# Kernel optimization log

Hardware: AMD Instinct MI355X
Metric: run time of the kernel (lower is better)

## Reference

```python
import math
import jax, jax.numpy as jnp
import numpy as np

B, N, E, H = 1, 4096, 256, 8
D = E // H  # head dim = 32


def setup_inputs() -> dict:
    key = jax.random.key(0)
    ks = jax.random.split(key, 10)
    s = 1.0 / math.sqrt(E)
    return {
        "x": jax.random.normal(ks[0], (B, N, E), dtype=jnp.float32),
        "adjacency": jax.random.randint(ks[1], (B, N, N), 0, 2, dtype=jnp.int32),
        "Wq": jax.random.normal(ks[2], (E, E), dtype=jnp.float32) * s,
        "bq": jnp.zeros((E,), dtype=jnp.float32),
        "Wk": jax.random.normal(ks[3], (E, E), dtype=jnp.float32) * s,
        "bk": jnp.zeros((E,), dtype=jnp.float32),
        "Wv": jax.random.normal(ks[4], (E, E), dtype=jnp.float32) * s,
        "bv": jnp.zeros((E,), dtype=jnp.float32),
        "Wo": jax.random.normal(ks[5], (E, E), dtype=jnp.float32) * s,
        "bo": jnp.zeros((E,), dtype=jnp.float32),
    }


def reference(x, adjacency, Wq, bq, Wk, bk, Wv, bv, Wo, bo):
    b, n, e = x.shape
    # projections (torch Linear: x @ W.T + b), split into heads -> [B,H,N,D]
    def heads(y):
        return y.reshape(b, n, H, D).transpose(0, 2, 1, 3)
    q = heads(x @ Wq.T + bq)
    k = heads(x @ Wk.T + bk)
    v = heads(x @ Wv.T + bv)
    scores = jnp.einsum("bhnd,bhmd->bhnm", q, k) / math.sqrt(D)
    mask = (adjacency[:, None, :, :] == 0)  # [B,1,N,N]
    scores = jnp.where(mask, -jnp.inf, scores)
    w = jax.nn.softmax(scores, axis=-1)
    out = jnp.einsum("bhnm,bhmd->bhnd", w, v)
    out = out.transpose(0, 2, 1, 3).reshape(b, n, e)
    return out @ Wo.T + bo
```

## Files before the change

kernel.cpp:

```cpp
#include <hip/hip_runtime.h>
#include <math.h>


#define NTOK 4096
#define EDIM 256
#define HEADS 8
#define HD 32
#define QSCALE 0.17677669529663687f
#define LOG2E 1.4426950408889634f
#define CINIT (-11.541560327111707f)

typedef __attribute__((ext_vector_type(8))) short bf16x8;
typedef __attribute__((ext_vector_type(4))) float f32x4;
typedef __attribute__((ext_vector_type(4))) unsigned long long u64x4;

static __device__ inline short f2bf(float f) {
    unsigned u = __float_as_uint(f);
    u = (u + 0x7FFFu + ((u >> 16) & 1u)) >> 16;
    return (short)u;
}
static __device__ inline unsigned packtrunc(float a, float b) {
    return __builtin_amdgcn_perm(__float_as_uint(b), __float_as_uint(a),
                                 0x07060302u);
}
static __device__ inline float sel_mask(float v, unsigned long long m) {
    float r;
    asm("v_cndmask_b32 %0, 0, %1, %2" : "=v"(r) : "v"(v), "s"(m));
    return r;
}

__global__ __launch_bounds__(256) void prep(
    const int* __restrict__ adj, unsigned long long* __restrict__ maskT,
    const float* __restrict__ x,  const float* __restrict__ Wq,
    const float* __restrict__ Wk, const float* __restrict__ Wv,
    const float* __restrict__ Wo,
    short* __restrict__ xb,  short* __restrict__ wqb,
    short* __restrict__ wkb, short* __restrict__ wvb,
    short* __restrict__ wob)
{
    const int bid = blockIdx.x;
    if (bid < 2048) {
        const int wb = bid * 4 + (threadIdx.x >> 6);
        const int l = threadIdx.x & 63;
        const int lrow = l & 15;
        const int lc4 = ((l >> 4) & 3) * 4;
#pragma unroll
        for (int i = 0; i < 8; ++i) {
            const int w = wb + i * 8192;
            const int qb = w >> 8;
            const int kt = (w >> 2) & 63;
            const int b = w & 3;
            const int row = qb * 16 + lrow;
            const int col = kt * 64 + b * 16 + lc4;
            const int4 av = *(const int4*)&adj[row * NTOK + col];
            const unsigned long long m0 = __ballot(av.x != 0);
            const unsigned long long m1 = __ballot(av.y != 0);
            const unsigned long long m2 = __ballot(av.z != 0);
            const unsigned long long m3 = __ballot(av.w != 0);
            if (l == 0) {
                unsigned long long* dst = &maskT[(size_t)w * 4];
                dst[0] = m0; dst[1] = m1; dst[2] = m2; dst[3] = m3;
            }
        }
    } else {
        const int gid = (bid - 2048) * 256 + threadIdx.x;
        const int e = gid * 4;
        const float* src; short* dst; int off;
        if (e < NTOK * EDIM) { src = x; dst = xb; off = e; }
        else {
            const int r = e - NTOK * EDIM;
            const int wsel = r >> 16;
            off = r & 65535;
            src = (wsel == 0) ? Wq : (wsel == 1) ? Wk : (wsel == 2) ? Wv : Wo;
            dst = (wsel == 0) ? wqb : (wsel == 1) ? wkb : (wsel == 2) ? wvb : wob;
        }
        float4 v = *(const float4*)&src[off];
        uint2 t;
        t.x = (unsigned short)f2bf(v.x) | ((unsigned)(unsigned short)f2bf(v.y) << 16);
        t.y = (unsigned short)f2bf(v.z) | ((unsigned)(unsigned short)f2bf(v.w) << 16);
        *(uint2*)&dst[off] = t;
    }
}

__global__ __launch_bounds__(256) void qkv_mfma(
    const short* __restrict__ xb,
    const short* __restrict__ Wqb, const short* __restrict__ Wkb,
    const short* __restrict__ Wvb,
    const float* __restrict__ bq, const float* __restrict__ bk,
    const float* __restrict__ bv,
    short* __restrict__ qo, short* __restrict__ ko, short* __restrict__ vto)
{
    const int tid = threadIdx.x;
    const int wv = tid >> 6, lane = tid & 63;
    const int grp = lane >> 4, lcol = lane & 15;
    const int wsel = blockIdx.y >> 2;
    const int n0 = (blockIdx.y & 3) << 6;
    const int m0 = blockIdx.x * 64 + wv * 16;
    const short* __restrict__ W = (wsel == 0) ? Wqb : (wsel == 1) ? Wkb : Wvb;
    const float* __restrict__ bias = (wsel == 0) ? bq : (wsel == 1) ? bk : bv;

    bf16x8 af[8];
#pragma unroll
    for (int k = 0; k < 8; ++k)
        af[k] = *(const bf16x8*)&xb[(m0 + lcol) * 256 + k * 32 + grp * 8];

    f32x4 acc[4] = {};
#pragma unroll
    for (int k = 0; k < 8; ++k) {
#pragma unroll
        for (int t = 0; t < 4; ++t) {
            const bf16x8 bt =
                *(const bf16x8*)&W[(n0 + t * 16 + lcol) * 256 + k * 32 + grp * 8];
            acc[t] = __builtin_amdgcn_mfma_f32_16x16x32_bf16(af[k], bt, acc[t], 0, 0, 0);
        }
    }
#pragma unroll
    for (int t = 0; t < 4; ++t) {
        const int feat = n0 + t * 16 + lcol;
        const float bval = bias[feat];
        const int h = feat >> 5, d = feat & 31;
        if (wsel == 2) {
            uint2 o;
            o.x = (unsigned short)f2bf(acc[t][0] + bval) |
                  ((unsigned)(unsigned short)f2bf(acc[t][1] + bval) << 16);
            o.y = (unsigned short)f2bf(acc[t][2] + bval) |
                  ((unsigned)(unsigned short)f2bf(acc[t][3] + bval) << 16);
            *(uint2*)&vto[h * (HD * NTOK) + d * NTOK + m0 + grp * 4] = o;
        } else {
            short* __restrict__ out = (wsel == 0) ? qo : ko;
            const float sc = (wsel == 0) ? (QSCALE * LOG2E) : 1.0f;
#pragma unroll
            for (int j = 0; j < 4; ++j)
                out[h * (NTOK * HD) + (m0 + grp * 4 + j) * HD + d] =
                    f2bf((acc[t][j] + bval) * sc);
        }
    }
}

__global__ __launch_bounds__(256) void attn_mfma(
    const short* __restrict__ qg, const short* __restrict__ kg,
    const short* __restrict__ vtg, const unsigned long long* __restrict__ maskT,
    float* __restrict__ o_part, float* __restrict__ l_part)
{
    const int h = blockIdx.y;
    const int split = blockIdx.z;
    const int q0 = blockIdx.x << 6;
    const short* __restrict__ Q  = qg  + h * (NTOK * HD);
    const short* __restrict__ K  = kg  + h * (NTOK * HD);
    const short* __restrict__ Vt = vtg + h * (HD * NTOK);

    __shared__ short Ks[2][64][40];
    __shared__ short Vs[2][32][72];
    __shared__ short P_lds[4][16][76];

    const int tid = threadIdx.x;
    const int wv = tid >> 6;
    const int lane = tid & 63;
    const int grp = lane >> 4;
    const int lcol = lane & 15;
    const int q0w = q0 + wv * 16;

    const int krow = tid >> 2, kc8 = (tid & 3) << 3;
    const int vrow = tid >> 3, vc8 = (tid & 7) << 3;

    const bf16x8 qfrag = *(const bf16x8*)&Q[(q0w + lcol) * HD + grp * 8];

    const int qb = __builtin_amdgcn_readfirstlane(blockIdx.x * 4 + wv);
    const unsigned long long* __restrict__ mbase = maskT + (size_t)qb * 1024;

    f32x4 ot[2] = {};
    f32x4 lacc = {};
    const f32x4 cinit = {CINIT, CINIT, CINIT, CINIT};
    bf16x8 ones;
#pragma unroll
    for (int i = 0; i < 8; ++i) ones[i] = (short)0x3F80;

    const int tps = 64 / (int)gridDim.z;
    const int kt_begin = split * tps;
    const int kt_end = kt_begin + tps;

    {
        const int k0 = kt_begin << 6;
        const int4 kr = *(const int4*)&K[(k0 + krow) * HD + kc8];
        const int4 vr = *(const int4*)&Vt[vrow * NTOK + k0 + vc8];
        *(int4*)&Ks[0][krow][kc8] = kr;
        *(int4*)&Vs[0][vrow][vc8] = vr;
    }
    __syncthreads();

    int cur = 0;
    for (int kt = kt_begin; kt < kt_end; ++kt) {
        int4 kr, vr;
        const bool has_next = (kt + 1 < kt_end);
        if (has_next) {
            const int k0n = (kt + 1) << 6;
            kr = *(const int4*)&K[(k0n + krow) * HD + kc8];
            vr = *(const int4*)&Vt[vrow * NTOK + k0n + vc8];
        }

        const u64x4* mp = (const u64x4*)(mbase + kt * 16);
        const u64x4 wa = mp[0], wb = mp[1], wc = mp[2], wd = mp[3];

        bf16x8 kf[4], vf[4];
#pragma unroll
        for (int b = 0; b < 4; ++b)
            kf[b] = *(const bf16x8*)&Ks[cur][b * 16 + lcol][grp * 8];
#pragma unroll
        for (int c = 0; c < 2; ++c) {
            vf[c * 2 + 0] = *(const bf16x8*)&Vs[cur][c * 16 + lcol][grp * 8];
            vf[c * 2 + 1] = *(const bf16x8*)&Vs[cur][c * 16 + lcol][32 + grp * 8];
        }

        f32x4 s[4];
        __builtin_amdgcn_s_setprio(1);
#pragma unroll
        for (int b = 0; b < 4; ++b)
            s[b] = __builtin_amdgcn_mfma_f32_16x16x32_bf16(
                kf[b], qfrag, cinit, 0, 0, 0);
        __builtin_amdgcn_s_setprio(0);

#pragma unroll
        for (int b = 0; b < 4; ++b) {
            const u64x4 wj = (b == 0) ? wa : (b == 1) ? wb : (b == 2) ? wc : wd;
            const float p0 = sel_mask(__builtin_amdgcn_exp2f(s[b][0]), wj[0]);
            const float p1 = sel_mask(__builtin_amdgcn_exp2f(s[b][1]), wj[1]);
            const float p2 = sel_mask(__builtin_amdgcn_exp2f(s[b][2]), wj[2]);
            const float p3 = sel_mask(__builtin_amdgcn_exp2f(s[b][3]), wj[3]);
            uint2 t;
            t.x = packtrunc(p0, p1);
            t.y = packtrunc(p2, p3);
            *(uint2*)&P_lds[wv][lcol][b * 16 + grp * 4] = t;
        }

        const uint2 pl0 = *(const uint2*)&P_lds[wv][lcol][grp * 8];
        const uint2 pl1 = *(const uint2*)&P_lds[wv][lcol][grp * 8 + 4];
        const uint2 pl2 = *(const uint2*)&P_lds[wv][lcol][32 + grp * 8];
        const uint2 pl3 = *(const uint2*)&P_lds[wv][lcol][32 + grp * 8 + 4];
        struct { uint2 a, b; } u0 = {pl0, pl1}, u1 = {pl2, pl3};
        const bf16x8 pf0 = __builtin_bit_cast(bf16x8, u0);
        const bf16x8 pf1 = __builtin_bit_cast(bf16x8, u1);

        __builtin_amdgcn_s_setprio(1);
#pragma unroll
        for (int c = 0; c < 2; ++c) {
            ot[c] = __builtin_amdgcn_mfma_f32_16x16x32_bf16(vf[c * 2 + 0], pf0, ot[c], 0, 0, 0);
            ot[c] = __builtin_amdgcn_mfma_f32_16x16x32_bf16(vf[c * 2 + 1], pf1, ot[c], 0, 0, 0);
        }
        lacc = __builtin_amdgcn_mfma_f32_16x16x32_bf16(ones, pf0, lacc, 0, 0, 0);
        lacc = __builtin_amdgcn_mfma_f32_16x16x32_bf16(ones, pf1, lacc, 0, 0, 0);
        __builtin_amdgcn_s_setprio(0);

        if (has_next) {
            *(int4*)&Ks[cur ^ 1][krow][kc8] = kr;
            *(int4*)&Vs[cur ^ 1][vrow][vc8] = vr;
        }
        __syncthreads();
        cur ^= 1;
    }

    float* __restrict__ ob = o_part + split * (NTOK * EDIM);
#pragma unroll
    for (int c = 0; c < 2; ++c) {
        float4 st;
        st.x = ot[c][0]; st.y = ot[c][1]; st.z = ot[c][2]; st.w = ot[c][3];
        *(float4*)&ob[(q0w + lcol) * EDIM + h * HD + c * 16 + grp * 4] = st;
    }
    if (grp == 0)
        l_part[split * (NTOK * HEADS) + (q0w + lcol) * HEADS + h] = lacc[0];
}

template <int NS>
__global__ __launch_bounds__(256) void out_mfma(
    const float* __restrict__ o_part, const float* __restrict__ l_part,
    const short* __restrict__ Wob, const float* __restrict__ bo,
    float* __restrict__ Y)
{
    const int tid = threadIdx.x;
    const int wv = tid >> 6, lane = tid & 63;
    const int grp = lane >> 4, lcol = lane & 15;
    const int n0 = blockIdx.y << 6;
    const int m0 = blockIdx.x * 64 + wv * 16;
    const int r = m0 + lcol;

    bf16x8 af[8];
#pragma unroll
    for (int k = 0; k < 8; ++k) {
        float4 s0 = {0.f, 0.f, 0.f, 0.f}, s1 = {0.f, 0.f, 0.f, 0.f};
        float lv = 0.f;
#pragma unroll
        for (int s = 0; s < NS; ++s) {
            const float* op = &o_part[s * (NTOK * EDIM) + r * EDIM + k * 32 + grp * 8];
            const float4 t0 = *(const float4*)op;
            const float4 t1 = *(const float4*)(op + 4);
            s0.x += t0.x; s0.y += t0.y; s0.z += t0.z; s0.w += t0.w;
            s1.x += t1.x; s1.y += t1.y; s1.z += t1.z; s1.w += t1.w;
            lv += l_part[s * (NTOK * HEADS) + r * HEADS + k];
        }
        const float inv = 1.0f / lv;
        bf16x8 t;
        t[0] = f2bf(s0.x * inv); t[1] = f2bf(s0.y * inv);
        t[2] = f2bf(s0.z * inv); t[3] = f2bf(s0.w * inv);
        t[4] = f2bf(s1.x * inv); t[5] = f2bf(s1.y * inv);
        t[6] = f2bf(s1.z * inv); t[7] = f2bf(s1.w * inv);
        af[k] = t;
    }

    f32x4 acc[4] = {};
#pragma unroll
    for (int k = 0; k < 8; ++k) {
#pragma unroll
        for (int t = 0; t < 4; ++t) {
            const bf16x8 bt =
                *(const bf16x8*)&Wob[(n0 + t * 16 + lcol) * 256 + k * 32 + grp * 8];
            acc[t] = __builtin_amdgcn_mfma_f32_16x16x32_bf16(af[k], bt, acc[t], 0, 0, 0);
        }
    }
#pragma unroll
    for (int t = 0; t < 4; ++t) {
        const float bval = bo[n0 + t * 16 + lcol];
#pragma unroll
        for (int j = 0; j < 4; ++j)
            Y[(m0 + grp * 4 + j) * EDIM + n0 + t * 16 + lcol] = acc[t][j] + bval;
    }
}

extern "C" void kernel_launch(void* const* d_in, const int* in_sizes, int n_in,
                              void* d_out, int out_size, void* d_ws, size_t ws_size,
                              hipStream_t stream) {
    (void)in_sizes; (void)n_in; (void)out_size;
    const float* x  = (const float*)d_in[0];
    const int*  adj = (const int*)d_in[1];
    const float* Wq = (const float*)d_in[2];
    const float* bq = (const float*)d_in[3];
    const float* Wk = (const float*)d_in[4];
    const float* bk = (const float*)d_in[5];
    const float* Wv = (const float*)d_in[6];
    const float* bv = (const float*)d_in[7];
    const float* Wo = (const float*)d_in[8];
    const float* bo = (const float*)d_in[9];

    char* ws = (char*)d_ws;
    short* x_bf  = (short*)(ws);
    short* q_ws  = (short*)(ws + (2u << 20));
    short* k_ws  = (short*)(ws + (4u << 20));
    short* vt_ws = (short*)(ws + (6u << 20));
    unsigned long long* maskT =
        (unsigned long long*)(ws + (8u << 20));
    short* Wq_bf = (short*)(ws + (10u << 20));
    short* Wk_bf = Wq_bf + (EDIM * EDIM);
    short* Wv_bf = Wk_bf + (EDIM * EDIM);
    short* Wo_bf = Wv_bf + (EDIM * EDIM);
    float* l_part = (float*)(ws + (11u << 20));
    float* o_part = (float*)(ws + (12u << 20));

    const int ns = (ws_size >= (28u << 20)) ? 4 : 2;

    prep<<<dim3(2048 + 1280), 256, 0, stream>>>(
        adj, maskT, x, Wq, Wk, Wv, Wo, x_bf, Wq_bf, Wk_bf, Wv_bf, Wo_bf);
    qkv_mfma<<<dim3(64, 12), 256, 0, stream>>>(x_bf, Wq_bf, Wk_bf, Wv_bf,
                                               bq, bk, bv, q_ws, k_ws, vt_ws);
    attn_mfma<<<dim3(64, HEADS, ns), 256, 0, stream>>>(
        q_ws, k_ws, vt_ws, maskT, o_part, l_part);
    if (ns == 4)
        out_mfma<4><<<dim3(64, 4), 256, 0, stream>>>(o_part, l_part, Wo_bf, bo,
                                                     (float*)d_out);
    else
        out_mfma<2><<<dim3(64, 4), 256, 0, stream>>>(o_part, l_part, Wo_bf, bo,
                                                     (float*)d_out);
}
```

Measured before the change: 183.6 us.

## Stage K/V tiles via direct global-to-LDS loads with XOR swizzle; fix split at 2

```diff
diff --git a/kernel.cpp b/kernel.cpp
--- a/kernel.cpp
+++ b/kernel.cpp
@@ -6,6 +6,7 @@
 #define EDIM 256
 #define HEADS 8
 #define HD 32
+#define NSPLIT 2
 #define QSCALE 0.17677669529663687f
 #define LOG2E 1.4426950408889634f
 #define CINIT (-11.541560327111707f)
@@ -13,6 +14,9 @@
 typedef __attribute__((ext_vector_type(8))) short bf16x8;
 typedef __attribute__((ext_vector_type(4))) float f32x4;
 typedef __attribute__((ext_vector_type(4))) unsigned long long u64x4;
+
+typedef __attribute__((address_space(3))) unsigned char lds_u8;
+typedef const __attribute__((address_space(1))) unsigned char gl_u8;
 
 static __device__ inline short f2bf(float f) {
     unsigned u = __float_as_uint(f);
@@ -149,8 +153,8 @@
     const short* __restrict__ K  = kg  + h * (NTOK * HD);
     const short* __restrict__ Vt = vtg + h * (HD * NTOK);
 
-    __shared__ short Ks[2][64][40];
-    __shared__ short Vs[2][32][72];
+    __shared__ short Ks[2][64][32];
+    __shared__ short Vs[2][32][64];
     __shared__ short P_lds[4][16][76];
 
     const int tid = threadIdx.x;
@@ -159,9 +163,13 @@
     const int grp = lane >> 4;
     const int lcol = lane & 15;
     const int q0w = q0 + wv * 16;
-
-    const int krow = tid >> 2, kc8 = (tid & 3) << 3;
-    const int vrow = tid >> 3, vc8 = (tid & 7) << 3;
+    const int wvu = __builtin_amdgcn_readfirstlane(wv);
+
+    const int k_row = tid >> 2, k_oct = tid & 3;
+    const int v_row = tid >> 3;
+    const int v_oct = (tid & 7) ^ (v_row & 7);
+    const short* __restrict__ kbase = &K[k_row * HD + k_oct * 8];
+    const short* __restrict__ vbase = &Vt[v_row * NTOK + v_oct * 8];
 
     const bf16x8 qfrag = *(const bf16x8*)&Q[(q0w + lcol) * HD + grp * 8];
 
@@ -179,24 +187,25 @@
     const int kt_begin = split * tps;
     const int kt_end = kt_begin + tps;
 
-    {
-        const int k0 = kt_begin << 6;
-        const int4 kr = *(const int4*)&K[(k0 + krow) * HD + kc8];
-        const int4 vr = *(const int4*)&Vt[vrow * NTOK + k0 + vc8];
-        *(int4*)&Ks[0][krow][kc8] = kr;
-        *(int4*)&Vs[0][vrow][vc8] = vr;
-    }
+#define STAGE(BUF, KT)                                                       \
+    {                                                                        \
+        const int k0s = (KT) << 6;                                           \
+        __builtin_amdgcn_global_load_lds(                                    \
+            (gl_u8*)(kbase + k0s * HD),                                      \
+            (lds_u8*)((unsigned char*)&Ks[BUF][0][0] + (wvu << 10)),         \
+            16, 0, 0);                                                       \
+        __builtin_amdgcn_global_load_lds(                                    \
+            (gl_u8*)(vbase + k0s),                                           \
+            (lds_u8*)((unsigned char*)&Vs[BUF][0][0] + (wvu << 10)),         \
+            16, 0, 0);                                                       \
+    }
+
+    STAGE(0, kt_begin)
     __syncthreads();
 
     int cur = 0;
     for (int kt = kt_begin; kt < kt_end; ++kt) {
-        int4 kr, vr;
-        const bool has_next = (kt + 1 < kt_end);
-        if (has_next) {
-            const int k0n = (kt + 1) << 6;
-            kr = *(const int4*)&K[(k0n + krow) * HD + kc8];
-            vr = *(const int4*)&Vt[vrow * NTOK + k0n + vc8];
-        }
+        if (kt + 1 < kt_end) STAGE(cur ^ 1, kt + 1)
 
         const u64x4* mp = (const u64x4*)(mbase + kt * 16);
         const u64x4 wa = mp[0], wb = mp[1], wc = mp[2], wd = mp[3];
@@ -207,8 +216,10 @@
             kf[b] = *(const bf16x8*)&Ks[cur][b * 16 + lcol][grp * 8];
 #pragma unroll
         for (int c = 0; c < 2; ++c) {
-            vf[c * 2 + 0] = *(const bf16x8*)&Vs[cur][c * 16 + lcol][grp * 8];
-            vf[c * 2 + 1] = *(const bf16x8*)&Vs[cur][c * 16 + lcol][32 + grp * 8];
+            vf[c * 2 + 0] =
+                *(const bf16x8*)&Vs[cur][c * 16 + lcol][(grp ^ (lcol & 7)) * 8];
+            vf[c * 2 + 1] =
+                *(const bf16x8*)&Vs[cur][c * 16 + lcol][((4 + grp) ^ (lcol & 7)) * 8];
         }
 
         f32x4 s[4];
@@ -250,13 +261,10 @@
         lacc = __builtin_amdgcn_mfma_f32_16x16x32_bf16(ones, pf1, lacc, 0, 0, 0);
         __builtin_amdgcn_s_setprio(0);
 
-        if (has_next) {
-            *(int4*)&Ks[cur ^ 1][krow][kc8] = kr;
-            *(int4*)&Vs[cur ^ 1][vrow][vc8] = vr;
-        }
         __syncthreads();
         cur ^= 1;
     }
+#undef STAGE
 
     float* __restrict__ ob = o_part + split * (NTOK * EDIM);
 #pragma unroll
@@ -327,7 +335,7 @@
 extern "C" void kernel_launch(void* const* d_in, const int* in_sizes, int n_in,
                               void* d_out, int out_size, void* d_ws, size_t ws_size,
                               hipStream_t stream) {
-    (void)in_sizes; (void)n_in; (void)out_size;
+    (void)in_sizes; (void)n_in; (void)out_size; (void)ws_size;
     const float* x  = (const float*)d_in[0];
     const int*  adj = (const int*)d_in[1];
     const float* Wq = (const float*)d_in[2];
@@ -353,18 +361,12 @@
     float* l_part = (float*)(ws + (11u << 20));
     float* o_part = (float*)(ws + (12u << 20));
 
-    const int ns = (ws_size >= (28u << 20)) ? 4 : 2;
-
     prep<<<dim3(2048 + 1280), 256, 0, stream>>>(
         adj, maskT, x, Wq, Wk, Wv, Wo, x_bf, Wq_bf, Wk_bf, Wv_bf, Wo_bf);
     qkv_mfma<<<dim3(64, 12), 256, 0, stream>>>(x_bf, Wq_bf, Wk_bf, Wv_bf,
                                                bq, bk, bv, q_ws, k_ws, vt_ws);
-    attn_mfma<<<dim3(64, HEADS, ns), 256, 0, stream>>>(
+    attn_mfma<<<dim3(64, HEADS, NSPLIT), 256, 0, stream>>>(
         q_ws, k_ws, vt_ws, maskT, o_part, l_part);
-    if (ns == 4)
-        out_mfma<4><<<dim3(64, 4), 256, 0, stream>>>(o_part, l_part, Wo_bf, bo,
-                                                     (float*)d_out);
-    else
-        out_mfma<2><<<dim3(64, 4), 256, 0, stream>>>(o_part, l_part, Wo_bf, bo,
-                                                     (float*)d_out);
-}
+    out_mfma<NSPLIT><<<dim3(64, 4), 256, 0, stream>>>(o_part, l_part, Wo_bf, bo,
+                                                      (float*)d_out);
+}
```

Result: faster. 177.1 us (-3.5%).
